# Kernel tuning notes

Hardware: AMD Instinct MI355X
Metric: run time of the kernel (lower is better)

## Reference

```python
import jax, jax.numpy as jnp
import numpy as np

B, L, C = 2, 2048, 1024
H = 16
D = C // H  # 64
MAX_SCALE_MUL = float(np.log(100.0))
EPS = 1e-12


def setup_inputs() -> dict:
    key = jax.random.key(0)
    ks = jax.random.split(key, 6)
    x = jax.random.normal(ks[0], (B, L, C), dtype=jnp.float32)
    attn_bias = jax.random.normal(ks[1], (1, 1, L, L), dtype=jnp.float32) * 0.02
    W_qkv = jax.random.normal(ks[2], (3 * C, C), dtype=jnp.float32) * (1.0 / np.sqrt(C))
    q_bias = jnp.zeros((C,), dtype=jnp.float32)
    v_bias = jnp.zeros((C,), dtype=jnp.float32)
    scale_mul = jnp.full((1, H, 1, 1), np.log(4.0), dtype=jnp.float32)
    W_proj = jax.random.normal(ks[3], (C, C), dtype=jnp.float32) * (1.0 / np.sqrt(C))
    b_proj = jnp.zeros((C,), dtype=jnp.float32)
    return {"x": x, "attn_bias": attn_bias, "W_qkv": W_qkv, "q_bias": q_bias,
            "v_bias": v_bias, "scale_mul": scale_mul, "W_proj": W_proj, "b_proj": b_proj}


def _l2norm(t):
    # F.normalize(dim=-1): x / max(||x||_2, eps)
    n = jnp.sqrt(jnp.sum(t * t, axis=-1, keepdims=True))
    return t / jnp.maximum(n, EPS)


def reference(x, attn_bias, W_qkv, q_bias, v_bias, scale_mul, W_proj, b_proj):
    bias = jnp.concatenate([q_bias, jnp.zeros_like(q_bias), v_bias])  # (3C,)
    qkv = x @ W_qkv.T + bias                     # (B, L, 3C)
    qkv = qkv.reshape(B, L, 3, H, D)
    q, k, v = jnp.moveaxis(qkv, 2, 0)            # each (B, L, H, D)
    q = jnp.transpose(q, (0, 2, 1, 3))           # (B, H, L, D)
    k = jnp.transpose(k, (0, 2, 1, 3))
    v = jnp.transpose(v, (0, 2, 1, 3))
    # attn_l2_norm path: scale = 1, learned per-head scale clamped at log(100)
    sm = jnp.exp(jnp.minimum(scale_mul, MAX_SCALE_MUL))  # (1, H, 1, 1)
    q = _l2norm(q) * sm
    k = _l2norm(k)
    scores = jnp.einsum('bhqd,bhkd->bhqk', q, k) + attn_bias  # scale=1
    attn = jax.nn.softmax(scores, axis=-1)
    out = jnp.einsum('bhqk,bhkd->bhqd', attn, v)  # (B, H, L, D)
    out = jnp.transpose(out, (0, 2, 1, 3)).reshape(B, L, C)
    return out @ W_proj.T + b_proj
```

## Files before the change

kernel.cpp:

```cpp
#include <hip/hip_runtime.h>


typedef __bf16 bf16x8 __attribute__((ext_vector_type(8)));
typedef __bf16 bf16x4 __attribute__((ext_vector_type(4)));
typedef float  f32x4  __attribute__((ext_vector_type(4)));

#define BB 2
#define LL 2048
#define CC 1024
#define HH 16
#define DD 64
#define LOG2E 1.44269504088896f

__device__ __forceinline__ f32x4 mfma_16x16x32(bf16x8 a, bf16x8 b, f32x4 c) {
    return __builtin_amdgcn_mfma_f32_16x16x32_bf16(a, b, c, 0, 0, 0);
}

__global__ __launch_bounds__(256) void cvt_bf16_kernel(const float* __restrict__ in,
                                                       __bf16* __restrict__ out, int n4) {
    int i = blockIdx.x * 256 + threadIdx.x;
    if (i >= n4) return;
    float4 v = reinterpret_cast<const float4*>(in)[i];
    bf16x4 o;
    o[0] = (__bf16)v.x; o[1] = (__bf16)v.y; o[2] = (__bf16)v.z; o[3] = (__bf16)v.w;
    reinterpret_cast<bf16x4*>(out)[i] = o;
}

__global__ __launch_bounds__(256) void bias_prep_kernel(const float* __restrict__ bias,
                                                        __bf16* __restrict__ bias_bf) {
    __shared__ float wmax[4];
    const int l = blockIdx.x, tid = threadIdx.x;
    const int w = tid >> 6;
    float4 a = reinterpret_cast<const float4*>(bias + (size_t)l * 2048)[tid];
    float4 b = reinterpret_cast<const float4*>(bias + (size_t)l * 2048 + 1024)[tid];
    float m = fmaxf(fmaxf(fmaxf(a.x, a.y), fmaxf(a.z, a.w)),
                    fmaxf(fmaxf(b.x, b.y), fmaxf(b.z, b.w)));
#pragma unroll
    for (int off = 1; off < 64; off <<= 1) m = fmaxf(m, __shfl_xor(m, off, 64));
    if ((tid & 63) == 0) wmax[w] = m;
    __syncthreads();
    float M = fmaxf(fmaxf(wmax[0], wmax[1]), fmaxf(wmax[2], wmax[3]));
    bf16x4 o0, o1;
    o0[0] = (__bf16)(a.x - M); o0[1] = (__bf16)(a.y - M);
    o0[2] = (__bf16)(a.z - M); o0[3] = (__bf16)(a.w - M);
    o1[0] = (__bf16)(b.x - M); o1[1] = (__bf16)(b.y - M);
    o1[2] = (__bf16)(b.z - M); o1[3] = (__bf16)(b.w - M);
    reinterpret_cast<bf16x4*>(bias_bf + (size_t)l * 2048)[tid] = o0;
    reinterpret_cast<bf16x4*>(bias_bf + (size_t)l * 2048 + 1024)[tid] = o1;
}

template <int OUT_MODE>
__global__ __launch_bounds__(256) void gemm_bt_kernel(
    const __bf16* __restrict__ A, const __bf16* __restrict__ Bm,
    float* __restrict__ Cf, __bf16* __restrict__ Cb,
    const float* __restrict__ bias, int M, int N, int K) {
    __shared__ __bf16 As[128 * 64];
    __shared__ __bf16 Bs[128 * 64];
    const int tid = threadIdx.x;
    const int m0 = blockIdx.x * 128, n0 = blockIdx.y * 128;
    const int w  = tid >> 6, l = tid & 63;
    const int wr = (w >> 1) * 64, wc = (w & 1) * 64;
    const int lr = l & 15, lg = l >> 4;
    const int rmask = (lr & 7) << 4;
    f32x4 acc[4][4] = {};
    const int srow = tid >> 1;
    const int scb  = (tid & 1) * 64;
    const int smask = (srow & 7) << 4;
    const __bf16* ag = A  + (size_t)(m0 + srow) * K + (tid & 1) * 32;
    const __bf16* bg = Bm + (size_t)(n0 + srow) * K + (tid & 1) * 32;
    char* asb = (char*)As + srow * 128;
    char* bsb = (char*)Bs + srow * 128;

    for (int kt = 0; kt < K; kt += 64) {
        bf16x8 av[4], bv[4];
#pragma unroll
        for (int j = 0; j < 4; ++j) {
            av[j] = *reinterpret_cast<const bf16x8*>(ag + kt + j * 8);
            bv[j] = *reinterpret_cast<const bf16x8*>(bg + kt + j * 8);
        }
        __syncthreads();
#pragma unroll
        for (int j = 0; j < 4; ++j) {
            *reinterpret_cast<bf16x8*>(asb + ((scb + j * 16) ^ smask)) = av[j];
            *reinterpret_cast<bf16x8*>(bsb + ((scb + j * 16) ^ smask)) = bv[j];
        }
        __syncthreads();
#pragma unroll
        for (int kk = 0; kk < 2; ++kk) {
            bf16x8 af[4], bfr[4];
#pragma unroll
            for (int m = 0; m < 4; ++m)
                af[m] = *reinterpret_cast<const bf16x8*>(
                    (char*)As + (wr + m * 16 + lr) * 128 + ((kk * 64 + lg * 16) ^ rmask));
#pragma unroll
            for (int n = 0; n < 4; ++n)
                bfr[n] = *reinterpret_cast<const bf16x8*>(
                    (char*)Bs + (wc + n * 16 + lr) * 128 + ((kk * 64 + lg * 16) ^ rmask));
#pragma unroll
            for (int m = 0; m < 4; ++m)
#pragma unroll
                for (int n = 0; n < 4; ++n)
                    acc[m][n] = mfma_16x16x32(af[m], bfr[n], acc[m][n]);
        }
    }
#pragma unroll
    for (int m = 0; m < 4; ++m) {
#pragma unroll
        for (int n = 0; n < 4; ++n) {
            const int row = m0 + wr + m * 16 + lg * 4;
            const int col = n0 + wc + n * 16 + lr;
#pragma unroll
            for (int r = 0; r < 4; ++r) {
                float v = acc[m][n][r];
                if (OUT_MODE == 0) {
                    Cb[(size_t)(row + r) * N + col] = (__bf16)v;
                } else {
                    Cf[(size_t)(row + r) * N + col] = v + bias[col];
                }
            }
        }
    }
}

__global__ __launch_bounds__(256) void qkv_norm_kernel(
    const __bf16* __restrict__ qkv, const float* __restrict__ q_bias,
    const float* __restrict__ v_bias, const float* __restrict__ scale_mul,
    __bf16* __restrict__ Q, __bf16* __restrict__ K, __bf16* __restrict__ V) {
    const int bl = blockIdx.x;
    const int tid = threadIdx.x;
    const int w = tid >> 6, d = tid & 63;
    const int b = bl >> 11, l = bl & 2047;
    for (int g = w; g < 48; g += 4) {
        const int s = g >> 4, h = g & 15;
        float v = (float)qkv[(size_t)bl * 3072 + g * 64 + d];
        if (s == 0) v += q_bias[h * 64 + d];
        if (s == 2) v += v_bias[h * 64 + d];
        if (s < 2) {
            float ss = v * v;
#pragma unroll
            for (int off = 1; off < 64; off <<= 1) ss += __shfl_xor(ss, off, 64);
            float nrm = sqrtf(ss);
            v = v / fmaxf(nrm, 1e-12f);
            if (s == 0) v *= __expf(fminf(scale_mul[h], 4.60517019f));
        }
        __bf16* dst = (s == 0) ? Q : ((s == 1) ? K : V);
        dst[((size_t)(b * 16 + h) * 2048 + l) * 64 + d] = (__bf16)v;
    }
}

__global__ __launch_bounds__(256) void v_transpose_kernel(const __bf16* __restrict__ Vin,
                                                          __bf16* __restrict__ Vt) {
    __shared__ __bf16 T[64][72];
    const int lb = blockIdx.x, bh = blockIdx.y;
    const int tid = threadIdx.x;
    const size_t base = (size_t)bh * LL * DD;
    const int row = tid >> 2, c = (tid & 3) * 16;
    {
        const __bf16* src = Vin + base + (size_t)(lb * 64 + row) * 64 + c;
        *reinterpret_cast<bf16x8*>(&T[row][c])     = *reinterpret_cast<const bf16x8*>(src);
        *reinterpret_cast<bf16x8*>(&T[row][c + 8]) = *reinterpret_cast<const bf16x8*>(src + 8);
    }
    __syncthreads();
    bf16x8 o0, o1;
#pragma unroll
    for (int j = 0; j < 8; ++j) {
        o0[j] = T[c + j][row];
        o1[j] = T[c + 8 + j][row];
    }
    __bf16* dst = Vt + base + (size_t)row * 2048 + lb * 64 + c;
    *reinterpret_cast<bf16x8*>(dst)     = o0;
    *reinterpret_cast<bf16x8*>(dst + 8) = o1;
}

__global__ __launch_bounds__(256) void attn_kernel(
    const __bf16* __restrict__ Q, const __bf16* __restrict__ K,
    const __bf16* __restrict__ Vt, const __bf16* __restrict__ bias_bf,
    const float* __restrict__ scale_mul, __bf16* __restrict__ Octx) {
    __shared__ __bf16 KVs[2][2][64 * 64];
    __shared__ __bf16 Ps[64 * 64];
    const int bh = blockIdx.x, qb = blockIdx.y;
    const int tid = threadIdx.x;
    const int w = tid >> 6, l = tid & 63;
    const int lr = l & 15, lg = l >> 4;
    const int rmask = (lr & 7) << 4;
    const int b = bh >> 4, h = bh & 15;
    const size_t base = (size_t)bh * LL * DD;
    const float smh = __expf(fminf(scale_mul[h], 4.60517019f));
    const float cexp = -smh * LOG2E;

    const int gq = qb * 64 + w * 16 + lr;
    bf16x8 qf[2];
    qf[0] = *reinterpret_cast<const bf16x8*>(Q + base + (size_t)gq * 64 + lg * 8);
    qf[1] = *reinterpret_cast<const bf16x8*>(Q + base + (size_t)gq * 64 + 32 + lg * 8);
    const __bf16* brow = bias_bf + (size_t)gq * 2048;

    const int srow = tid >> 2;
    const int scb  = (tid & 3) * 32;
    const int smask = (srow & 7) << 4;
    const __bf16* kgbase = K  + base + (size_t)srow * 64   + (tid & 3) * 16;
    const __bf16* vgbase = Vt + base + (size_t)srow * 2048 + (tid & 3) * 16;

    bf16x8 k0, k1, v0, v1;
    auto stage_regs = [&](int kb) {
        const __bf16* kg = kgbase + (size_t)kb * 64 * 64;
        k0 = *reinterpret_cast<const bf16x8*>(kg);
        k1 = *reinterpret_cast<const bf16x8*>(kg + 8);
        const __bf16* vg = vgbase + kb * 64;
        v0 = *reinterpret_cast<const bf16x8*>(vg);
        v1 = *reinterpret_cast<const bf16x8*>(vg + 8);
    };
    auto write_lds = [&](int buf) {
        char* kp = (char*)KVs[buf][0] + srow * 128;
        char* vp = (char*)KVs[buf][1] + srow * 128;
        *reinterpret_cast<bf16x8*>(kp + (scb ^ smask))        = k0;
        *reinterpret_cast<bf16x8*>(kp + ((scb + 16) ^ smask)) = k1;
        *reinterpret_cast<bf16x8*>(vp + (scb ^ smask))        = v0;
        *reinterpret_cast<bf16x8*>(vp + ((scb + 16) ^ smask)) = v1;
    };

    stage_regs(0);
    write_lds(0);

    f32x4 Oa[4] = {};
    float lsum = 0.f;
    int cur = 0;
    char* psb = (char*)Ps + (w * 16 + lr) * 128;

    for (int kb = 0; kb < 32; ++kb) {
        __syncthreads();
        if (kb < 31) stage_regs(kb + 1);

        const char* Kc = (const char*)KVs[cur][0];
        const char* Vc = (const char*)KVs[cur][1];

        f32x4 sa[4] = {};
#pragma unroll
        for (int t = 0; t < 4; ++t) {
            const char* kr = Kc + (t * 16 + lr) * 128;
            bf16x8 kf0 = *reinterpret_cast<const bf16x8*>(kr + ((lg * 16) ^ rmask));
            bf16x8 kf1 = *reinterpret_cast<const bf16x8*>(kr + ((64 + lg * 16) ^ rmask));
            sa[t] = mfma_16x16x32(kf0, qf[0], sa[t]);
            sa[t] = mfma_16x16x32(kf1, qf[1], sa[t]);
        }

#pragma unroll
        for (int t = 0; t < 4; ++t) {
            bf16x4 bv = *reinterpret_cast<const bf16x4*>(brow + kb * 64 + t * 16 + lg * 4);
            bf16x4 pb;
#pragma unroll
            for (int r = 0; r < 4; ++r) {
                float s = sa[t][r] + (float)bv[r];
                float p = exp2f(fmaf(s, LOG2E, cexp));
                lsum += p;
                pb[r] = (__bf16)p;
            }
            *reinterpret_cast<bf16x4*>(psb + ((t * 32 + lg * 8) ^ rmask)) = pb;
        }

        bf16x8 pf0 = *reinterpret_cast<const bf16x8*>(psb + ((lg * 16) ^ rmask));
        bf16x8 pf1 = *reinterpret_cast<const bf16x8*>(psb + ((64 + lg * 16) ^ rmask));
#pragma unroll
        for (int t = 0; t < 4; ++t) {
            const char* vr = Vc + (t * 16 + lr) * 128;
            bf16x8 vf0 = *reinterpret_cast<const bf16x8*>(vr + ((lg * 16) ^ rmask));
            bf16x8 vf1 = *reinterpret_cast<const bf16x8*>(vr + ((64 + lg * 16) ^ rmask));
            Oa[t] = mfma_16x16x32(pf0, vf0, Oa[t]);
            Oa[t] = mfma_16x16x32(pf1, vf1, Oa[t]);
        }

        if (kb < 31) write_lds(cur ^ 1);
        cur ^= 1;
    }

    lsum += __shfl_xor(lsum, 16, 64);
    lsum += __shfl_xor(lsum, 32, 64);
    float inv[4];
#pragma unroll
    for (int r = 0; r < 4; ++r) inv[r] = 1.0f / __shfl(lsum, lg * 4 + r, 64);

#pragma unroll
    for (int t = 0; t < 4; ++t)
#pragma unroll
        for (int r = 0; r < 4; ++r) {
            const int row = qb * 64 + w * 16 + lg * 4 + r;
            float o = Oa[t][r] * inv[r];
            Octx[((size_t)(b * 2048 + row)) * 1024 + h * 64 + t * 16 + lr] = (__bf16)o;
        }
}

extern "C" void kernel_launch(void* const* d_in, const int* in_sizes, int n_in,
                              void* d_out, int out_size, void* d_ws, size_t ws_size,
                              hipStream_t stream) {
    const float* x         = (const float*)d_in[0];
    const float* attn_bias = (const float*)d_in[1];
    const float* W_qkv     = (const float*)d_in[2];
    const float* q_bias    = (const float*)d_in[3];
    const float* v_bias    = (const float*)d_in[4];
    const float* scale_mul = (const float*)d_in[5];
    const float* W_proj    = (const float*)d_in[6];
    const float* b_proj    = (const float*)d_in[7];
    float* out = (float*)d_out;

    char* ws = (char*)d_ws;
    size_t off = 0;
    auto alloc = [&](size_t bytes) {
        void* p = ws + off;
        off = (off + bytes + 255) & ~(size_t)255;
        return p;
    };
    __bf16* xb     = (__bf16*)alloc((size_t)4096 * 1024 * 2);
    __bf16* wqkvb  = (__bf16*)alloc((size_t)3072 * 1024 * 2);
    __bf16* wprojb = (__bf16*)alloc((size_t)1024 * 1024 * 2);
    __bf16* qkvb   = (__bf16*)alloc((size_t)4096 * 3072 * 2);
    __bf16* Qw     = (__bf16*)alloc((size_t)BB * HH * LL * DD * 2);
    __bf16* Kw     = (__bf16*)alloc((size_t)BB * HH * LL * DD * 2);
    __bf16* Vw     = (__bf16*)alloc((size_t)BB * HH * LL * DD * 2);
    __bf16* Oc     = (__bf16*)alloc((size_t)4096 * 1024 * 2);
    __bf16* bias_bf = qkvb;
    __bf16* Vt      = qkvb + (size_t)2048 * 2048;

    cvt_bf16_kernel<<<4096, 256, 0, stream>>>(x, xb, 4096 * 1024 / 4);
    cvt_bf16_kernel<<<3072, 256, 0, stream>>>(W_qkv, wqkvb, 3072 * 1024 / 4);
    cvt_bf16_kernel<<<1024, 256, 0, stream>>>(W_proj, wprojb, 1024 * 1024 / 4);

    gemm_bt_kernel<0><<<dim3(32, 24), 256, 0, stream>>>(
        xb, wqkvb, nullptr, qkvb, nullptr, 4096, 3072, 1024);

    qkv_norm_kernel<<<4096, 256, 0, stream>>>(qkvb, q_bias, v_bias, scale_mul, Qw, Kw, Vw);

    bias_prep_kernel<<<2048, 256, 0, stream>>>(attn_bias, bias_bf);
    v_transpose_kernel<<<dim3(32, 32), 256, 0, stream>>>(Vw, Vt);

    attn_kernel<<<dim3(32, 32), 256, 0, stream>>>(Qw, Kw, Vt, bias_bf, scale_mul, Oc);

    gemm_bt_kernel<1><<<dim3(32, 8), 256, 0, stream>>>(
        Oc, wprojb, out, nullptr, b_proj, 4096, 1024, 1024);
}
```

Baseline: 196.9 us.

## Use direct global-to-LDS loads in GEMM and attention, shuffle P via lanes

Replaces register-staged global loads followed by LDS stores with global_load_lds direct-to-LDS transfers in both the GEMM and attention kernels, using a swizzle in the global address to keep the XOR layout. In attention, the P tile no longer round-trips through shared memory; it is packed to bf16 pairs and redistributed across lanes with shuffles to form the MFMA A operand. Bias values for the next block are prefetched into registers. This cuts VGPR pressure, LDS traffic and the extra LDS buffer, at the cost of many cross-lane shuffles and a full vmcnt wait each iteration, and relies on the direct-load lane layout being correct.

```diff
diff --git a/kernel.cpp b/kernel.cpp
--- a/kernel.cpp
+++ b/kernel.cpp
@@ -14,6 +14,19 @@
 
 __device__ __forceinline__ f32x4 mfma_16x16x32(bf16x8 a, bf16x8 b, f32x4 c) {
     return __builtin_amdgcn_mfma_f32_16x16x32_bf16(a, b, c, 0, 0, 0);
+}
+
+__device__ __forceinline__ void gload_lds16(const __bf16* g, __bf16* lds) {
+    __builtin_amdgcn_global_load_lds(
+        (const __attribute__((address_space(1))) unsigned int*)g,
+        (__attribute__((address_space(3))) unsigned int*)lds,
+        16, 0, 0);
+}
+
+__device__ __forceinline__ unsigned pk_bf16(float a, float b) {
+    unsigned short ua = __builtin_bit_cast(unsigned short, (__bf16)a);
+    unsigned short ub = __builtin_bit_cast(unsigned short, (__bf16)b);
+    return (unsigned)ua | ((unsigned)ub << 16);
 }
 
 __global__ __launch_bounds__(256) void cvt_bf16_kernel(const float* __restrict__ in,
@@ -63,27 +76,18 @@
     const int lr = l & 15, lg = l >> 4;
     const int rmask = (lr & 7) << 4;
     f32x4 acc[4][4] = {};
-    const int srow = tid >> 1;
-    const int scb  = (tid & 1) * 64;
-    const int smask = (srow & 7) << 4;
-    const __bf16* ag = A  + (size_t)(m0 + srow) * K + (tid & 1) * 32;
-    const __bf16* bg = Bm + (size_t)(n0 + srow) * K + (tid & 1) * 32;
-    char* asb = (char*)As + srow * 128;
-    char* bsb = (char*)Bs + srow * 128;
+    const int lrow = l >> 3;
+    const int celem = (((l & 7) ^ lrow) << 3);
 
     for (int kt = 0; kt < K; kt += 64) {
-        bf16x8 av[4], bv[4];
-#pragma unroll
-        for (int j = 0; j < 4; ++j) {
-            av[j] = *reinterpret_cast<const bf16x8*>(ag + kt + j * 8);
-            bv[j] = *reinterpret_cast<const bf16x8*>(bg + kt + j * 8);
-        }
         __syncthreads();
 #pragma unroll
-        for (int j = 0; j < 4; ++j) {
-            *reinterpret_cast<bf16x8*>(asb + ((scb + j * 16) ^ smask)) = av[j];
-            *reinterpret_cast<bf16x8*>(bsb + ((scb + j * 16) ^ smask)) = bv[j];
-        }
+        for (int i = 0; i < 4; ++i) {
+            const int row = w * 32 + i * 8;
+            gload_lds16(A + (size_t)(m0 + row + lrow) * K + kt + celem, &As[row * 64]);
+            gload_lds16(Bm + (size_t)(n0 + row + lrow) * K + kt + celem, &Bs[row * 64]);
+        }
+        asm volatile("s_waitcnt vmcnt(0)" ::: "memory");
         __syncthreads();
 #pragma unroll
         for (int kk = 0; kk < 2; ++kk) {
@@ -177,7 +181,6 @@
     const __bf16* __restrict__ Vt, const __bf16* __restrict__ bias_bf,
     const float* __restrict__ scale_mul, __bf16* __restrict__ Octx) {
     __shared__ __bf16 KVs[2][2][64 * 64];
-    __shared__ __bf16 Ps[64 * 64];
     const int bh = blockIdx.x, qb = blockIdx.y;
     const int tid = threadIdx.x;
     const int w = tid >> 6, l = tid & 63;
@@ -194,41 +197,42 @@
     qf[1] = *reinterpret_cast<const bf16x8*>(Q + base + (size_t)gq * 64 + 32 + lg * 8);
     const __bf16* brow = bias_bf + (size_t)gq * 2048;
 
-    const int srow = tid >> 2;
-    const int scb  = (tid & 3) * 32;
-    const int smask = (srow & 7) << 4;
-    const __bf16* kgbase = K  + base + (size_t)srow * 64   + (tid & 3) * 16;
-    const __bf16* vgbase = Vt + base + (size_t)srow * 2048 + (tid & 3) * 16;
-
-    bf16x8 k0, k1, v0, v1;
-    auto stage_regs = [&](int kb) {
-        const __bf16* kg = kgbase + (size_t)kb * 64 * 64;
-        k0 = *reinterpret_cast<const bf16x8*>(kg);
-        k1 = *reinterpret_cast<const bf16x8*>(kg + 8);
-        const __bf16* vg = vgbase + kb * 64;
-        v0 = *reinterpret_cast<const bf16x8*>(vg);
-        v1 = *reinterpret_cast<const bf16x8*>(vg + 8);
+    const int lrow = l >> 3;
+    const int celem = (((l & 7) ^ lrow) << 3);
+    auto stage = [&](int buf, int kb) {
+        __bf16* Kd = &KVs[buf][0][0];
+        __bf16* Vd = &KVs[buf][1][0];
+#pragma unroll
+        for (int i = 0; i < 2; ++i) {
+            const int row = w * 16 + i * 8;
+            gload_lds16(K  + base + ((size_t)kb * 64 + row + lrow) * 64 + celem, Kd + row * 64);
+            gload_lds16(Vt + base + (size_t)(row + lrow) * 2048 + kb * 64 + celem, Vd + row * 64);
+        }
     };
-    auto write_lds = [&](int buf) {
-        char* kp = (char*)KVs[buf][0] + srow * 128;
-        char* vp = (char*)KVs[buf][1] + srow * 128;
-        *reinterpret_cast<bf16x8*>(kp + (scb ^ smask))        = k0;
-        *reinterpret_cast<bf16x8*>(kp + ((scb + 16) ^ smask)) = k1;
-        *reinterpret_cast<bf16x8*>(vp + (scb ^ smask))        = v0;
-        *reinterpret_cast<bf16x8*>(vp + ((scb + 16) ^ smask)) = v1;
-    };
-
-    stage_regs(0);
-    write_lds(0);
+
+    stage(0, 0);
+    asm volatile("s_waitcnt vmcnt(0)" ::: "memory");
 
     f32x4 Oa[4] = {};
     float lsum = 0.f;
     int cur = 0;
-    char* psb = (char*)Ps + (w * 16 + lr) * 128;
+    bf16x4 bcur[4];
+#pragma unroll
+    for (int t = 0; t < 4; ++t)
+        bcur[t] = *reinterpret_cast<const bf16x4*>(brow + t * 16 + lg * 4);
+
+    const int sAx = lr + ((lg & 1) << 5);
+    const int sBx = sAx + 16;
 
     for (int kb = 0; kb < 32; ++kb) {
         __syncthreads();
-        if (kb < 31) stage_regs(kb + 1);
+        if (kb < 31) stage(cur ^ 1, kb + 1);
+        bf16x4 bnext[4];
+        if (kb < 31) {
+#pragma unroll
+            for (int t = 0; t < 4; ++t)
+                bnext[t] = *reinterpret_cast<const bf16x4*>(brow + (kb + 1) * 64 + t * 16 + lg * 4);
+        }
 
         const char* Kc = (const char*)KVs[cur][0];
         const char* Vc = (const char*)KVs[cur][1];
@@ -243,32 +247,53 @@
             sa[t] = mfma_16x16x32(kf1, qf[1], sa[t]);
         }
 
+        unsigned wv[4][2];
 #pragma unroll
         for (int t = 0; t < 4; ++t) {
-            bf16x4 bv = *reinterpret_cast<const bf16x4*>(brow + kb * 64 + t * 16 + lg * 4);
-            bf16x4 pb;
+            float pv[4];
 #pragma unroll
             for (int r = 0; r < 4; ++r) {
-                float s = sa[t][r] + (float)bv[r];
-                float p = exp2f(fmaf(s, LOG2E, cexp));
-                lsum += p;
-                pb[r] = (__bf16)p;
+                float s = sa[t][r] + (float)bcur[t][r];
+                pv[r] = exp2f(fmaf(s, LOG2E, cexp));
+                lsum += pv[r];
             }
-            *reinterpret_cast<bf16x4*>(psb + ((t * 32 + lg * 8) ^ rmask)) = pb;
-        }
-
-        bf16x8 pf0 = *reinterpret_cast<const bf16x8*>(psb + ((lg * 16) ^ rmask));
-        bf16x8 pf1 = *reinterpret_cast<const bf16x8*>(psb + ((64 + lg * 16) ^ rmask));
+            wv[t][0] = pk_bf16(pv[0], pv[1]);
+            wv[t][1] = pk_bf16(pv[2], pv[3]);
+        }
+
+        int e0  = __shfl((int)wv[0][0], sAx, 64), e1  = __shfl((int)wv[0][1], sAx, 64);
+        int e2  = __shfl((int)wv[0][0], sBx, 64), e3  = __shfl((int)wv[0][1], sBx, 64);
+        int e4  = __shfl((int)wv[1][0], sAx, 64), e5  = __shfl((int)wv[1][1], sAx, 64);
+        int e6  = __shfl((int)wv[1][0], sBx, 64), e7  = __shfl((int)wv[1][1], sBx, 64);
+        int e8  = __shfl((int)wv[2][0], sAx, 64), e9  = __shfl((int)wv[2][1], sAx, 64);
+        int e10 = __shfl((int)wv[2][0], sBx, 64), e11 = __shfl((int)wv[2][1], sBx, 64);
+        int e12 = __shfl((int)wv[3][0], sAx, 64), e13 = __shfl((int)wv[3][1], sAx, 64);
+        int e14 = __shfl((int)wv[3][0], sBx, 64), e15 = __shfl((int)wv[3][1], sBx, 64);
+        const bool hi2 = (lg & 2) != 0;
+        union Upa { unsigned u[4]; bf16x8 v; } pa0, pa1;
+        pa0.u[0] = hi2 ? (unsigned)e4  : (unsigned)e0;
+        pa0.u[1] = hi2 ? (unsigned)e5  : (unsigned)e1;
+        pa0.u[2] = hi2 ? (unsigned)e6  : (unsigned)e2;
+        pa0.u[3] = hi2 ? (unsigned)e7  : (unsigned)e3;
+        pa1.u[0] = hi2 ? (unsigned)e12 : (unsigned)e8;
+        pa1.u[1] = hi2 ? (unsigned)e13 : (unsigned)e9;
+        pa1.u[2] = hi2 ? (unsigned)e14 : (unsigned)e10;
+        pa1.u[3] = hi2 ? (unsigned)e15 : (unsigned)e11;
+
 #pragma unroll
         for (int t = 0; t < 4; ++t) {
             const char* vr = Vc + (t * 16 + lr) * 128;
             bf16x8 vf0 = *reinterpret_cast<const bf16x8*>(vr + ((lg * 16) ^ rmask));
             bf16x8 vf1 = *reinterpret_cast<const bf16x8*>(vr + ((64 + lg * 16) ^ rmask));
-            Oa[t] = mfma_16x16x32(pf0, vf0, Oa[t]);
-            Oa[t] = mfma_16x16x32(pf1, vf1, Oa[t]);
-        }
-
-        if (kb < 31) write_lds(cur ^ 1);
+            Oa[t] = mfma_16x16x32(pa0.v, vf0, Oa[t]);
+            Oa[t] = mfma_16x16x32(pa1.v, vf1, Oa[t]);
+        }
+
+        if (kb < 31) {
+            asm volatile("s_waitcnt vmcnt(0)" ::: "memory");
+#pragma unroll
+            for (int t = 0; t < 4; ++t) bcur[t] = bnext[t];
+        }
         cur ^= 1;
     }
 
```

New measurement: 200.5 us. Within noise of the previous version (+1.8%).
